# Kernel optimization log

Hardware: AMD Instinct MI355X
Metric: run time of the kernel (lower is better)

## Reference

```python
import jax, jax.numpy as jnp
import numpy as np
from jax import lax

C = 64      # embed_dim
DI = 128    # d_inner (expand=2)
N = 16      # d_state
RK = 4      # dt_rank = ceil(C/16)
K = 4       # scan directions
NB = 8      # total VSS blocks (4 stages x 2)


def conv2d(x, w, b, stride=1, pad=1, groups=1):
    y = lax.conv_general_dilated(x, w, (stride, stride), [(pad, pad), (pad, pad)],
                                 dimension_numbers=('NCHW', 'OIHW', 'NCHW'),
                                 feature_group_count=groups)
    return y + b[None, :, None, None]


def ln2d(x, g, b, eps=1e-6):
    xt = x.transpose(0, 2, 3, 1)
    mu = xt.mean(-1, keepdims=True)
    var = ((xt - mu) ** 2).mean(-1, keepdims=True)
    y = (xt - mu) / jnp.sqrt(var + eps) * g + b
    return y.transpose(0, 3, 1, 2)


def selective_scan(u, delta, A, Bm, Cm, D):
    # u, delta: (B,K,d,L); A: (K,d,n); Bm, Cm: (B,K,n,L); D: (K,d)
    dA = jnp.exp(delta[..., None] * A[None, :, :, None, :])               # (B,K,d,L,n)
    dBu = delta[..., None] * Bm.transpose(0, 1, 3, 2)[:, :, None] * u[..., None]

    def comb(c1, c2):
        a1, b1 = c1
        a2, b2 = c2
        return a2 * a1, a2 * b1 + b2

    _, h = lax.associative_scan(comb, (dA, dBu), axis=3)                  # (B,K,d,L,n)
    y = jnp.einsum('bkdln,bkln->bkdl', h, Cm.transpose(0, 1, 3, 2))
    return y + D[None, :, :, None] * u


def vss_block(x, lg, lb, inw, cw, cb, xpw, dtw, dtb, a_log, dp, ong, onb, outw):
    B, _, H, W = x.shape
    L = H * W
    h = ln2d(x, lg, lb)
    xz = jnp.einsum('bchw,ce->behw', h, inw)                              # (B,2*DI,H,W)
    xc, z = xz[:, :DI], xz[:, DI:]
    xc = jax.nn.silu(conv2d(xc, cw, cb, groups=DI))                       # depthwise 3x3
    x1 = xc.reshape(B, DI, L)                                             # row-major
    x2 = xc.transpose(0, 1, 3, 2).reshape(B, DI, L)                       # col-major
    xs = jnp.stack([x1, x2, x1[..., ::-1], x2[..., ::-1]], axis=1)        # (B,K,DI,L)
    xdbl = jnp.einsum('bkdl,krd->bkrl', xs, xpw)
    dts, Bs, Cs = xdbl[:, :, :RK], xdbl[:, :, RK:RK + N], xdbl[:, :, RK + N:]
    delta = jax.nn.softplus(jnp.einsum('bkrl,kdr->bkdl', dts, dtw) + dtb[None, :, :, None])
    A = -jnp.exp(a_log)
    ys = selective_scan(xs, delta, A, Bs, Cs, dp)                         # (B,K,DI,L)
    y = (ys[:, 0].reshape(B, DI, H, W)
         + ys[:, 1].reshape(B, DI, W, H).transpose(0, 1, 3, 2)
         + ys[:, 2, :, ::-1].reshape(B, DI, H, W)
         + ys[:, 3, :, ::-1].reshape(B, DI, W, H).transpose(0, 1, 3, 2))
    yt = y.transpose(0, 2, 3, 1)
    mu = yt.mean(-1, keepdims=True)
    var = ((yt - mu) ** 2).mean(-1, keepdims=True)
    yt = (yt - mu) / jnp.sqrt(var + 1e-6) * ong + onb
    yt = yt * jax.nn.silu(z.transpose(0, 2, 3, 1))
    out = jnp.einsum('bhwd,dc->bhwc', yt, outw).transpose(0, 3, 1, 2)
    return x + out


def setup_inputs() -> dict:
    key = jax.random.key(0)
    ks = jax.random.split(key, 16)
    nrm = lambda k, s, sc=0.02: jax.random.normal(k, s, jnp.float32) * sc
    return dict(
        E0=jax.random.uniform(ks[0], (1, 1, 256, 256), jnp.float32),
        pe_w=nrm(ks[1], (C, 1, 4, 4), 0.1),
        pe_b=jnp.zeros((C,), jnp.float32),
        pe_lg=jnp.ones((C,), jnp.float32),
        pe_lb=jnp.zeros((C,), jnp.float32),
        ln_g=jnp.ones((NB, C), jnp.float32),
        ln_b=jnp.zeros((NB, C), jnp.float32),
        in_w=nrm(ks[2], (NB, C, 2 * DI)),
        cv_w=nrm(ks[3], (NB, DI, 1, 3, 3), 0.1),
        cv_b=jnp.zeros((NB, DI), jnp.float32),
        xp_w=nrm(ks[4], (NB, K, RK + 2 * N, DI)),
        dt_w=nrm(ks[5], (NB, K, DI, RK)),
        dt_b=nrm(ks[6], (NB, K, DI), 0.5),
        A_log=jnp.broadcast_to(jnp.log(jnp.arange(1., N + 1)), (NB, K, DI, N)).astype(jnp.float32),
        Dp=jnp.ones((NB, K, DI), jnp.float32),
        on_g=jnp.ones((NB, DI), jnp.float32),
        on_b=jnp.zeros((NB, DI), jnp.float32),
        out_pw=nrm(ks[7], (NB, DI, C)),
        dn_w=nrm(ks[8], (3, C, C, 3, 3), 0.05),
        dn_b=jnp.zeros((3, C), jnp.float32),
        dn_g=jnp.ones((3, C), jnp.float32),
        dn_lb=jnp.zeros((3, C), jnp.float32),
        up_w=nrm(ks[9], (3, C, C, 3, 3), 0.05),
        up_b=jnp.zeros((3, C), jnp.float32),
        oc_w=nrm(ks[10], (C, C, 3, 3), 0.05),
        oc_b=jnp.zeros((C,), jnp.float32),
    )


def reference(E0, pe_w, pe_b, pe_lg, pe_lb, ln_g, ln_b, in_w, cv_w, cv_b, xp_w,
              dt_w, dt_b, A_log, Dp, on_g, on_b, out_pw, dn_w, dn_b, dn_g, dn_lb,
              up_w, up_b, oc_w, oc_b):
    x = conv2d(E0, pe_w, pe_b, stride=4, pad=0)
    x = ln2d(x, pe_lg, pe_lb)
    skips = []
    cur = 0
    for i in range(4):
        for _ in range(2):
            x = vss_block(x, ln_g[cur], ln_b[cur], in_w[cur], cv_w[cur], cv_b[cur],
                          xp_w[cur], dt_w[cur], dt_b[cur], A_log[cur], Dp[cur],
                          on_g[cur], on_b[cur], out_pw[cur])
            cur += 1
        skips.append(x)
        if i < 3:
            x = ln2d(conv2d(x, dn_w[i], dn_b[i], stride=2), dn_g[i], dn_lb[i])
    for i in range(3):
        Bq, Cq, Hq, Wq = x.shape
        x = jax.image.resize(x, (Bq, Cq, Hq * 2, Wq * 2), method='bilinear')
        x = jax.nn.silu(conv2d(x, up_w[i], up_b[i]))
        x = x + skips[-(i + 2)]
    Bq, Cq, Hq, Wq = x.shape
    x = jax.image.resize(x, (Bq, Cq, Hq * 4, Wq * 4), method='bilinear')
    x = jax.nn.silu(conv2d(x, oc_w, oc_b))
    return x
```

## Files before the change

kernel.cpp:

```cpp
#include <hip/hip_runtime.h>
#include <hip/hip_bf16.h>
#include <utility>

__global__ void k_patch_embed_ln(const float* __restrict__ E0, const float* __restrict__ w,
                                 const float* __restrict__ b, const float* __restrict__ g,
                                 const float* __restrict__ lb, float* __restrict__ out) {
  int p = blockIdx.x;
  int c = threadIdx.x;
  int oh = p >> 6, ow = p & 63;
  const float* src = E0 + (oh * 4) * 256 + ow * 4;
  const float* wc = w + c * 16;
  float acc = b[c];
#pragma unroll
  for (int i = 0; i < 4; i++)
#pragma unroll
    for (int j = 0; j < 4; j++) acc += src[i * 256 + j] * wc[i * 4 + j];
  float s = acc, s2 = acc * acc;
#pragma unroll
  for (int m = 32; m >= 1; m >>= 1) {
    s += __shfl_xor(s, m, 64);
    s2 += __shfl_xor(s2, m, 64);
  }
  float mu = s * (1.f / 64.f);
  float var = s2 * (1.f / 64.f) - mu * mu;
  float rstd = rsqrtf(var + 1e-6f);
  out[c * 4096 + p] = (acc - mu) * rstd * g[c] + lb[c];
}

__global__ void k_ln2d64(const float* __restrict__ x, const float* __restrict__ g,
                         const float* __restrict__ b, float* __restrict__ y, int HW) {
  int p = blockIdx.x;
  int c = threadIdx.x;
  float v = x[c * HW + p];
  float s = v, s2 = v * v;
#pragma unroll
  for (int m = 32; m >= 1; m >>= 1) {
    s += __shfl_xor(s, m, 64);
    s2 += __shfl_xor(s2, m, 64);
  }
  float mu = s * (1.f / 64.f);
  float var = s2 * (1.f / 64.f) - mu * mu;
  float rstd = rsqrtf(var + 1e-6f);
  y[c * HW + p] = (v - mu) * rstd * g[c] + b[c];
}

__global__ void k_lnproj(const float* __restrict__ x, const float* __restrict__ g,
                         const float* __restrict__ b, const float* __restrict__ w,
                         float* __restrict__ xc, float* __restrict__ z, int HW) {
  int p = blockIdx.x;
  int t = threadIdx.x;
  __shared__ float hsh[64];
  if (t < 64) {
    float v = x[t * HW + p];
    float s = v, s2 = v * v;
#pragma unroll
    for (int m = 32; m >= 1; m >>= 1) {
      s += __shfl_xor(s, m, 64);
      s2 += __shfl_xor(s2, m, 64);
    }
    float mu = s * (1.f / 64.f);
    float var = s2 * (1.f / 64.f) - mu * mu;
    float rstd = rsqrtf(var + 1e-6f);
    hsh[t] = (v - mu) * rstd * g[t] + b[t];
  }
  __syncthreads();
  float acc = 0.f;
  const float* wp = w + t;
#pragma unroll
  for (int c = 0; c < 64; c++) acc += hsh[c] * wp[c * 256];
  if (t < 128)
    xc[(size_t)p * 128 + t] = acc;
  else
    z[(size_t)p * 128 + (t - 128)] = acc;
}

__global__ void k_dwconv(const float* __restrict__ xc, const float* __restrict__ w,
                         const float* __restrict__ b, float* __restrict__ out, int H, int lgH) {
  int HW = H * H;
  int idx = blockIdx.x * blockDim.x + threadIdx.x;
  if (idx >= 128 * HW) return;
  int p = idx >> 7;
  int d = idx & 127;
  int ph = p >> lgH, pw = p & (H - 1);
  const float* wp = w + d * 9;
  float acc = b[d];
#pragma unroll
  for (int i = 0; i < 3; i++) {
    int ih = ph + i - 1;
    if (ih < 0 || ih >= H) continue;
#pragma unroll
    for (int j = 0; j < 3; j++) {
      int iw = pw + j - 1;
      if (iw < 0 || iw >= H) continue;
      acc += xc[(size_t)(ih * H + iw) * 128 + d] * wp[i * 3 + j];
    }
  }
  out[(size_t)p * 128 + d] = acc / (1.f + __expf(-acc));
}

__global__ void k_xproj(const float* __restrict__ xcs, const float* __restrict__ xpw,
                        const float* __restrict__ dtw, const float* __restrict__ dtb,
                        float* __restrict__ delta, float* __restrict__ Bs,
                        float* __restrict__ Cs, int H, int lgH) {
  int L = H * H;
  int l = blockIdx.x;
  int k = blockIdx.y;
  int t = threadIdx.x;
  int lm = (k & 2) ? (L - 1 - l) : l;
  int idx = (k & 1) ? ((lm & (H - 1)) * H + (lm >> lgH)) : lm;
  __shared__ float xs[128];
  __shared__ float part[36][4];
  __shared__ float r4[4];
  if (t < 128) xs[t] = xcs[(size_t)idx * 128 + t];
  __syncthreads();
  if (t < 144) {
    int r = t >> 2, q = t & 3;
    const float* wr = xpw + (k * 36 + r) * 128 + q * 32;
    const float* xp = xs + q * 32;
    float acc = 0.f;
#pragma unroll
    for (int c = 0; c < 32; c++) acc += xp[c] * wr[c];
    part[r][q] = acc;
  }
  __syncthreads();
  if (t < 36) {
    float acc = part[t][0] + part[t][1] + part[t][2] + part[t][3];
    if (t < 4)
      r4[t] = acc;
    else if (t < 20)
      Bs[((size_t)k * L + l) * 16 + (t - 4)] = acc;
    else
      Cs[((size_t)k * L + l) * 16 + (t - 20)] = acc;
  }
  __syncthreads();
  if (t < 128) {
    float dt = dtb[k * 128 + t];
    const float* wd = dtw + (k * 128 + t) * 4;
    dt += r4[0] * wd[0] + r4[1] * wd[1] + r4[2] * wd[2] + r4[3] * wd[3];
    float sp = fmaxf(dt, 0.f) + log1pf(__expf(-fabsf(dt)));
    delta[((size_t)k * L + l) * 128 + t] = sp;
  }
}

__global__ void k_scanA(const float* __restrict__ xcs, const float* __restrict__ delta,
                        const float* __restrict__ Bs, const float* __restrict__ A_log,
                        float* __restrict__ hloc, float* __restrict__ pA, int H, int lgH,
                        int nc, int cs) {
  int L = H * H;
  int c = blockIdx.x;
  int k = blockIdx.y;
  int d = threadIdx.x;
  float A[16], h[16];
#pragma unroll
  for (int n = 0; n < 16; n++) {
    A[n] = -expf(A_log[(k * 128 + d) * 16 + n]);
    h[n] = 0.f;
  }
  float sumdt = 0.f;
  int l0 = c * cs;
  for (int l = l0; l < l0 + cs; l++) {
    int lm = (k & 2) ? (L - 1 - l) : l;
    int idx = (k & 1) ? ((lm & (H - 1)) * H + (lm >> lgH)) : lm;
    float u = xcs[(size_t)idx * 128 + d];
    float dt = delta[((size_t)k * L + l) * 128 + d];
    float du = dt * u;
    sumdt += dt;
    const float4* bp = (const float4*)(Bs + ((size_t)k * L + l) * 16);
    float4 B0 = bp[0], B1 = bp[1], B2 = bp[2], B3 = bp[3];
    float Bv[16] = {B0.x, B0.y, B0.z, B0.w, B1.x, B1.y, B1.z, B1.w,
                    B2.x, B2.y, B2.z, B2.w, B3.x, B3.y, B3.z, B3.w};
#pragma unroll
    for (int n = 0; n < 16; n++) h[n] = __expf(dt * A[n]) * h[n] + Bv[n] * du;
  }
  size_t base = (((size_t)(k * 128 + d)) * nc + c) * 16;
#pragma unroll
  for (int n = 0; n < 16; n++) {
    hloc[base + n] = h[n];
    pA[base + n] = __expf(A[n] * sumdt);
  }
}

__global__ void k_scanB(const float* __restrict__ hloc, const float* __restrict__ pA,
                        float* __restrict__ hinit, int nc) {
  int tid = blockIdx.x * blockDim.x + threadIdx.x;
  int k = tid >> 11;
  int d = (tid >> 4) & 127;
  int n = tid & 15;
  size_t rb = ((size_t)(k * 128 + d)) * nc * 16 + n;
  float h = 0.f;
  for (int c = 0; c < nc; c++) {
    size_t a = rb + (size_t)c * 16;
    hinit[a] = h;
    h = pA[a] * h + hloc[a];
  }
}

__global__ void k_scanC(const float* __restrict__ xcs, const float* __restrict__ delta,
                        const float* __restrict__ Bs, const float* __restrict__ Cs,
                        const float* __restrict__ A_log, const float* __restrict__ Dp,
                        const float* __restrict__ hinit, float* __restrict__ ys, int H,
                        int lgH, int nc, int cs) {
  int L = H * H;
  int c = blockIdx.x;
  int k = blockIdx.y;
  int d = threadIdx.x;
  float A[16], h[16];
  size_t base = (((size_t)(k * 128 + d)) * nc + c) * 16;
#pragma unroll
  for (int n = 0; n < 16; n++) {
    A[n] = -expf(A_log[(k * 128 + d) * 16 + n]);
    h[n] = hinit[base + n];
  }
  float Dv = Dp[k * 128 + d];
  int l0 = c * cs;
  for (int l = l0; l < l0 + cs; l++) {
    int lm = (k & 2) ? (L - 1 - l) : l;
    int idx = (k & 1) ? ((lm & (H - 1)) * H + (lm >> lgH)) : lm;
    float u = xcs[(size_t)idx * 128 + d];
    float dt = delta[((size_t)k * L + l) * 128 + d];
    float du = dt * u;
    const float4* bp = (const float4*)(Bs + ((size_t)k * L + l) * 16);
    float4 B0 = bp[0], B1 = bp[1], B2 = bp[2], B3 = bp[3];
    float Bv[16] = {B0.x, B0.y, B0.z, B0.w, B1.x, B1.y, B1.z, B1.w,
                    B2.x, B2.y, B2.z, B2.w, B3.x, B3.y, B3.z, B3.w};
    const float4* cp = (const float4*)(Cs + ((size_t)k * L + l) * 16);
    float4 C0 = cp[0], C1 = cp[1], C2 = cp[2], C3 = cp[3];
    float Cv[16] = {C0.x, C0.y, C0.z, C0.w, C1.x, C1.y, C1.z, C1.w,
                    C2.x, C2.y, C2.z, C2.w, C3.x, C3.y, C3.z, C3.w};
    float y = 0.f;
#pragma unroll
    for (int n = 0; n < 16; n++) {
      h[n] = __expf(dt * A[n]) * h[n] + Bv[n] * du;
      y += h[n] * Cv[n];
    }
    ys[((size_t)k * L + l) * 128 + d] = y + Dv * u;
  }
}

__global__ void k_combine(const float* __restrict__ ys, const float* __restrict__ z,
                          const float* __restrict__ xin, const float* __restrict__ ong,
                          const float* __restrict__ onb, const float* __restrict__ outw,
                          float* __restrict__ xout, int H, int lgH) {
  int L = H * H;
  int p = blockIdx.x;
  int d = threadIdx.x;
  int ph = p >> lgH, pw = p & (H - 1);
  int l1 = pw * H + ph;
  float yv = ys[((size_t)0 * L + p) * 128 + d] + ys[((size_t)1 * L + l1) * 128 + d] +
             ys[((size_t)2 * L + (L - 1 - p)) * 128 + d] +
             ys[((size_t)3 * L + (L - 1 - l1)) * 128 + d];
  float s = yv, s2 = yv * yv;
#pragma unroll
  for (int m = 32; m >= 1; m >>= 1) {
    s += __shfl_xor(s, m, 64);
    s2 += __shfl_xor(s2, m, 64);
  }
  __shared__ float ws1[2], ws2[2];
  int wid = d >> 6;
  if ((d & 63) == 0) {
    ws1[wid] = s;
    ws2[wid] = s2;
  }
  __syncthreads();
  float tot = ws1[0] + ws1[1], tot2 = ws2[0] + ws2[1];
  float mu = tot * (1.f / 128.f);
  float var = tot2 * (1.f / 128.f) - mu * mu;
  float rstd = rsqrtf(var + 1e-6f);
  float zt = z[(size_t)p * 128 + d];
  float yt = ((yv - mu) * rstd * ong[d] + onb[d]) * (zt / (1.f + __expf(-zt)));
  __shared__ float ysm[128];
  ysm[d] = yt;
  __syncthreads();
  if (d < 64) {
    float acc = xin[(size_t)d * L + p];
#pragma unroll
    for (int q = 0; q < 128; q++) acc += ysm[q] * outw[q * 64 + d];
    xout[(size_t)d * L + p] = acc;
  }
}

__global__ void k_combine_lnproj(const float* __restrict__ ys, const float* __restrict__ z,
                                 const float* __restrict__ xin, const float* __restrict__ ong,
                                 const float* __restrict__ onb, const float* __restrict__ outw,
                                 const float* __restrict__ g2, const float* __restrict__ b2,
                                 const float* __restrict__ w2, float* __restrict__ xout,
                                 float* __restrict__ xc, float* __restrict__ zout, int H,
                                 int lgH) {
  int L = H * H;
  int p = blockIdx.x;
  int t = threadIdx.x;
  __shared__ float ysm[128], hnsh[64];
  __shared__ float ws1[2], ws2[2];
  float yv = 0.f;
  if (t < 128) {
    int ph = p >> lgH, pw = p & (H - 1);
    int l1 = pw * H + ph;
    yv = ys[((size_t)0 * L + p) * 128 + t] + ys[((size_t)1 * L + l1) * 128 + t] +
         ys[((size_t)2 * L + (L - 1 - p)) * 128 + t] +
         ys[((size_t)3 * L + (L - 1 - l1)) * 128 + t];
    float s = yv, s2 = yv * yv;
#pragma unroll
    for (int m = 32; m >= 1; m >>= 1) {
      s += __shfl_xor(s, m, 64);
      s2 += __shfl_xor(s2, m, 64);
    }
    if ((t & 63) == 0) {
      ws1[t >> 6] = s;
      ws2[t >> 6] = s2;
    }
  }
  __syncthreads();
  if (t < 128) {
    float tot = ws1[0] + ws1[1], tot2 = ws2[0] + ws2[1];
    float mu = tot * (1.f / 128.f);
    float var = tot2 * (1.f / 128.f) - mu * mu;
    float rstd = rsqrtf(var + 1e-6f);
    float zt = z[(size_t)p * 128 + t];
    ysm[t] = ((yv - mu) * rstd * ong[t] + onb[t]) * (zt / (1.f + __expf(-zt)));
  }
  __syncthreads();
  if (t < 64) {
    float acc = xin[(size_t)t * L + p];
#pragma unroll
    for (int q = 0; q < 128; q++) acc += ysm[q] * outw[q * 64 + t];
    xout[(size_t)t * L + p] = acc;
    float s = acc, s2 = acc * acc;
#pragma unroll
    for (int m = 32; m >= 1; m >>= 1) {
      s += __shfl_xor(s, m, 64);
      s2 += __shfl_xor(s2, m, 64);
    }
    float mu = s * (1.f / 64.f);
    float var = s2 * (1.f / 64.f) - mu * mu;
    float rstd = rsqrtf(var + 1e-6f);
    hnsh[t] = (acc - mu) * rstd * g2[t] + b2[t];
  }
  __syncthreads();
  float a2 = 0.f;
  const float* wp = w2 + t;
#pragma unroll
  for (int c = 0; c < 64; c++) a2 += hnsh[c] * wp[c * 256];
  if (t < 128)
    xc[(size_t)p * 128 + t] = a2;
  else
    zout[(size_t)p * 128 + (t - 128)] = a2;
}

__global__ void k_conv_naive(const float* __restrict__ x, const float* __restrict__ w,
                             const float* __restrict__ b, const float* __restrict__ skip,
                             float* __restrict__ out, int Hin, int Hout, int stride,
                             int do_silu) {
  int idx = blockIdx.x * blockDim.x + threadIdx.x;
  int HWo = Hout * Hout;
  if (idx >= 64 * HWo) return;
  int co = idx / HWo;
  int p = idx - co * HWo;
  int oh = p / Hout, ow = p - (p / Hout) * Hout;
  float acc = b[co];
  const float* wb = w + co * 64 * 9;
  for (int ci = 0; ci < 64; ci++) {
    const float* xb = x + (size_t)ci * Hin * Hin;
    const float* wc = wb + ci * 9;
#pragma unroll
    for (int i = 0; i < 3; i++) {
      int ih = oh * stride + i - 1;
      if (ih < 0 || ih >= Hin) continue;
#pragma unroll
      for (int j = 0; j < 3; j++) {
        int iw = ow * stride + j - 1;
        if (iw < 0 || iw >= Hin) continue;
        acc += xb[ih * Hin + iw] * wc[i * 3 + j];
      }
    }
  }
  if (do_silu) acc = acc / (1.f + __expf(-acc));
  if (skip) acc += skip[idx];
  out[idx] = acc;
}

__global__ void __launch_bounds__(256) k_conv16_up(const float* __restrict__ x,
                                                   const float* __restrict__ w,
                                                   const float* __restrict__ b,
                                                   float* __restrict__ out) {
  __shared__ __align__(16) float xsh[16][18][20];
  __shared__ __align__(16) float wsh[16][16][12];
  int t = threadIdx.x;
  int q = t & 63, cog = t >> 6;
  int qx = q & 7, qy = q >> 3;
  int ox = blockIdx.x * 16, oy = blockIdx.y * 16;
  int z16 = blockIdx.z * 16;
  float acc[4][4];
#pragma unroll
  for (int pp = 0; pp < 4; pp++)
#pragma unroll
    for (int i = 0; i < 4; i++) acc[pp][i] = 0.f;
  for (int cb = 0; cb < 64; cb += 16) {
    for (int i = t; i < 16 * 324; i += 256) {
      int ci = i / 324;
      int r = i - ci * 324;
      int iy = r / 18, ix = r - (r / 18) * 18;
      int gy = oy + iy - 1, gx = ox + ix - 1;
      float v = 0.f;
      if ((unsigned)gy < 256u && (unsigned)gx < 256u) {
        float sh = gy * 0.25f - 0.375f;
        float sw = gx * 0.25f - 0.375f;
        int h0 = (int)floorf(sh);
        float fh = sh - h0;
        int w0 = (int)floorf(sw);
        float fw = sw - w0;
        int h0c = max(h0, 0), h1c = min(h0 + 1, 63);
        int w0c = max(w0, 0), w1c = min(w0 + 1, 63);
        const float* xb = x + (size_t)(cb + ci) * 4096;
        v = (1.f - fh) * ((1.f - fw) * xb[h0c * 64 + w0c] + fw * xb[h0c * 64 + w1c]) +
            fh * ((1.f - fw) * xb[h1c * 64 + w0c] + fw * xb[h1c * 64 + w1c]);
      }
      xsh[ci][iy][ix] = v;
    }
    for (int i = t; i < 16 * 144; i += 256) {
      int ci = i / 144;
      int r = i - ci * 144;
      int col = r / 9, tap = r - (r / 9) * 9;
      wsh[ci][col][tap] = w[(size_t)(z16 + col) * 576 + (cb + ci) * 9 + tap];
    }
    __syncthreads();
#pragma unroll
    for (int ci = 0; ci < 16; ci++) {
      float xv[4][4];
#pragma unroll
      for (int r = 0; r < 4; r++) {
        float2 a = *(const float2*)&xsh[ci][2 * qy + r][2 * qx];
        float2 bq = *(const float2*)&xsh[ci][2 * qy + r][2 * qx + 2];
        xv[r][0] = a.x;
        xv[r][1] = a.y;
        xv[r][2] = bq.x;
        xv[r][3] = bq.y;
      }
#pragma unroll
      for (int i = 0; i < 4; i++) {
        int col = cog * 4 + i;
        float4 w0 = *(const float4*)&wsh[ci][col][0];
        float4 w1 = *(const float4*)&wsh[ci][col][4];
        float w8 = wsh[ci][col][8];
#pragma unroll
        for (int dy = 0; dy < 2; dy++)
#pragma unroll
          for (int dx = 0; dx < 2; dx++) {
            acc[dy * 2 + dx][i] += xv[dy + 0][dx + 0] * w0.x + xv[dy + 0][dx + 1] * w0.y +
                                   xv[dy + 0][dx + 2] * w0.z + xv[dy + 1][dx + 0] * w0.w +
                                   xv[dy + 1][dx + 1] * w1.x + xv[dy + 1][dx + 2] * w1.y +
                                   xv[dy + 2][dx + 0] * w1.z + xv[dy + 2][dx + 1] * w1.w +
                                   xv[dy + 2][dx + 2] * w8;
          }
      }
    }
    __syncthreads();
  }
#pragma unroll
  for (int dy = 0; dy < 2; dy++)
#pragma unroll
    for (int dx = 0; dx < 2; dx++) {
      int gy = oy + 2 * qy + dy, gx = ox + 2 * qx + dx;
#pragma unroll
      for (int i = 0; i < 4; i++) {
        int co = z16 + cog * 4 + i;
        float a = acc[dy * 2 + dx][i] + b[co];
        a = a / (1.f + __expf(-a));
        out[(size_t)co * 65536 + gy * 256 + gx] = a;
      }
    }
}

__global__ void k_resize(const float* __restrict__ x, float* __restrict__ out, int Hin,
                         int Win, int Hout, int Wout, float inv_scale) {
  int idx = blockIdx.x * blockDim.x + threadIdx.x;
  int HWo = Hout * Wout;
  if (idx >= 64 * HWo) return;
  int c = idx / HWo;
  int p = idx - c * HWo;
  int oh = p / Wout, ow = p - (p / Wout) * Wout;
  float sh = (oh + 0.5f) * inv_scale - 0.5f;
  float sw = (ow + 0.5f) * inv_scale - 0.5f;
  int h0 = (int)floorf(sh);
  float fh = sh - h0;
  int w0 = (int)floorf(sw);
  float fw = sw - w0;
  int h0c = min(max(h0, 0), Hin - 1), h1c = min(max(h0 + 1, 0), Hin - 1);
  int w0c = min(max(w0, 0), Win - 1), w1c = min(max(w0 + 1, 0), Win - 1);
  const float* xb = x + (size_t)c * Hin * Win;
  float v = (1.f - fh) * ((1.f - fw) * xb[h0c * Win + w0c] + fw * xb[h0c * Win + w1c]) +
            fh * ((1.f - fw) * xb[h1c * Win + w0c] + fw * xb[h1c * Win + w1c]);
  out[idx] = v;
}

extern "C" void kernel_launch(void* const* d_in, const int* in_sizes, int n_in, void* d_out,
                              int out_size, void* d_ws, size_t ws_size, hipStream_t stream) {
  const float* E0 = (const float*)d_in[0];
  const float* pe_w = (const float*)d_in[1];
  const float* pe_b = (const float*)d_in[2];
  const float* pe_lg = (const float*)d_in[3];
  const float* pe_lb = (const float*)d_in[4];
  const float* ln_g = (const float*)d_in[5];
  const float* ln_b = (const float*)d_in[6];
  const float* in_w = (const float*)d_in[7];
  const float* cv_w = (const float*)d_in[8];
  const float* cv_b = (const float*)d_in[9];
  const float* xp_w = (const float*)d_in[10];
  const float* dt_w = (const float*)d_in[11];
  const float* dt_b = (const float*)d_in[12];
  const float* A_log = (const float*)d_in[13];
  const float* Dp = (const float*)d_in[14];
  const float* on_g = (const float*)d_in[15];
  const float* on_b = (const float*)d_in[16];
  const float* out_pw = (const float*)d_in[17];
  const float* dn_w = (const float*)d_in[18];
  const float* dn_b = (const float*)d_in[19];
  const float* dn_g = (const float*)d_in[20];
  const float* dn_lb = (const float*)d_in[21];
  const float* up_w = (const float*)d_in[22];
  const float* up_b = (const float*)d_in[23];
  const float* oc_w = (const float*)d_in[24];
  const float* oc_b = (const float*)d_in[25];

  float* ws = (float*)d_ws;
  size_t off = 0;
  auto alloc = [&](size_t n) {
    float* p = ws + off;
    off += n;
    return p;
  };
  float* xA = alloc(64 * 4096);
  float* xB = alloc(64 * 4096);
  float* xc = alloc(128 * 4096);
  float* zb = alloc(128 * 4096);
  float* xcs = alloc(128 * 4096);
  float* dlt = alloc((size_t)4 * 128 * 4096);
  float* Bsb = alloc(4 * 16 * 4096);
  float* Csb = alloc(4 * 16 * 4096);
  float* ysb = alloc((size_t)4 * 128 * 4096);
  float* hloc = alloc((size_t)4 * 128 * 128 * 16);
  float* pAb = alloc((size_t)4 * 128 * 128 * 16);
  float* hin = alloc((size_t)4 * 128 * 128 * 16);
  float* sk0 = alloc(64 * 4096);
  float* sk1 = alloc(64 * 1024);
  float* sk2 = alloc(64 * 256);
  float* sk3 = alloc(64 * 64);
  float* tmpR = alloc((size_t)64 * 4096);

  k_patch_embed_ln<<<4096, 64, 0, stream>>>(E0, pe_w, pe_b, pe_lg, pe_lb, xB);
  float* x = xB;
  float* xalt = xA;

  int Hs[4] = {64, 32, 16, 8};
  int lgHs[4] = {6, 5, 4, 3};
  int CSs[4] = {32, 16, 8, 8};
  float* skips[4] = {sk0, sk1, sk2, sk3};
  int cur = 0;

  auto vss_core = [&](int H, int lgH, int cs) {
    int L = H * H;
    int nc = L / cs;
    k_dwconv<<<(128 * L + 255) / 256, 256, 0, stream>>>(xc, cv_w + (size_t)cur * 128 * 9,
                                                        cv_b + cur * 128, xcs, H, lgH);
    dim3 gx(L, 4);
    k_xproj<<<gx, 256, 0, stream>>>(xcs, xp_w + (size_t)cur * 4 * 36 * 128,
                                    dt_w + (size_t)cur * 4 * 128 * 4, dt_b + cur * 4 * 128,
                                    dlt, Bsb, Csb, H, lgH);
    const float* Al = A_log + (size_t)cur * 4 * 128 * 16;
    const float* Dv = Dp + cur * 4 * 128;
    dim3 ga(nc, 4);
    k_scanA<<<ga, 128, 0, stream>>>(xcs, dlt, Bsb, Al, hloc, pAb, H, lgH, nc, cs);
    k_scanB<<<32, 256, 0, stream>>>(hloc, pAb, hin, nc);
    k_scanC<<<ga, 128, 0, stream>>>(xcs, dlt, Bsb, Csb, Al, Dv, hin, ysb, H, lgH, nc, cs);
  };

  for (int i = 0; i < 4; i++) {
    int H = Hs[i], lgH = lgHs[i];
    int L = H * H;
    k_lnproj<<<L, 256, 0, stream>>>(x, ln_g + cur * 64, ln_b + cur * 64,
                                    in_w + (size_t)cur * 64 * 256, xc, zb, L);
    vss_core(H, lgH, CSs[i]);
    k_combine_lnproj<<<L, 256, 0, stream>>>(
        ysb, zb, x, on_g + cur * 128, on_b + cur * 128, out_pw + (size_t)cur * 128 * 64,
        ln_g + (cur + 1) * 64, ln_b + (cur + 1) * 64, in_w + (size_t)(cur + 1) * 64 * 256,
        xalt, xc, zb, H, lgH);
    std::swap(x, xalt);
    cur++;
    vss_core(H, lgH, CSs[i]);
    if (i < 3) {
      k_combine<<<L, 128, 0, stream>>>(ysb, zb, x, on_g + cur * 128, on_b + cur * 128,
                                       out_pw + (size_t)cur * 128 * 64, skips[i], H, lgH);
      cur++;
      int Ho = H / 2;
      k_conv_naive<<<(64 * Ho * Ho + 255) / 256, 256, 0, stream>>>(
          skips[i], dn_w + (size_t)i * 64 * 64 * 9, dn_b + i * 64, nullptr, xalt, H, Ho, 2, 0);
      k_ln2d64<<<Ho * Ho, 64, 0, stream>>>(xalt, dn_g + i * 64, dn_lb + i * 64, x, Ho * Ho);
    } else {
      k_combine<<<L, 128, 0, stream>>>(ysb, zb, x, on_g + cur * 128, on_b + cur * 128,
                                       out_pw + (size_t)cur * 128 * 64, xalt, H, lgH);
      std::swap(x, xalt);
      cur++;
    }
  }

  for (int i = 0; i < 3; i++) {
    int Hin = 8 << i, Ho = Hin * 2;
    k_resize<<<(64 * Ho * Ho + 255) / 256, 256, 0, stream>>>(x, tmpR, Hin, Hin, Ho, Ho, 0.5f);
    k_conv_naive<<<(64 * Ho * Ho + 255) / 256, 256, 0, stream>>>(
        tmpR, up_w + (size_t)i * 64 * 64 * 9, up_b + i * 64, skips[2 - i], xalt, Ho, Ho, 1, 1);
    std::swap(x, xalt);
  }

  dim3 gf(16, 16, 4);
  k_conv16_up<<<gf, 256, 0, stream>>>(x, oc_w, oc_b, (float*)d_out);
}
```

Before: 1.352 ms.

## Fuse x-projection into scan pass A and restructure final upsample conv

The per-position x-projection/softplus kernel is merged into the chunked scan pass A. Each block stages its chunk of inputs in shared memory, computes B, C and delta there and runs the local scan directly from shared memory, which removes a launch and the global round-trip of delta and B. The final 4x-upsample+conv kernel now stages a 6x6 source patch per channel and precomputes bilinear offsets and weights once. It also computes 32 output channels per block instead of 16, halving the grid. The trade-offs are fewer blocks, serial per-position syncs inside the fused kernel and more registers per thread in the conv.

Result: faster. 1.230 ms (-9.1%).

```diff
diff --git a/kernel.cpp b/kernel.cpp
--- a/kernel.cpp
+++ b/kernel.cpp
@@ -98,85 +98,100 @@
   out[(size_t)p * 128 + d] = acc / (1.f + __expf(-acc));
 }
 
-__global__ void k_xproj(const float* __restrict__ xcs, const float* __restrict__ xpw,
-                        const float* __restrict__ dtw, const float* __restrict__ dtb,
-                        float* __restrict__ delta, float* __restrict__ Bs,
-                        float* __restrict__ Cs, int H, int lgH) {
-  int L = H * H;
-  int l = blockIdx.x;
-  int k = blockIdx.y;
-  int t = threadIdx.x;
-  int lm = (k & 2) ? (L - 1 - l) : l;
-  int idx = (k & 1) ? ((lm & (H - 1)) * H + (lm >> lgH)) : lm;
-  __shared__ float xs[128];
-  __shared__ float part[36][4];
-  __shared__ float r4[4];
-  if (t < 128) xs[t] = xcs[(size_t)idx * 128 + t];
-  __syncthreads();
-  if (t < 144) {
-    int r = t >> 2, q = t & 3;
-    const float* wr = xpw + (k * 36 + r) * 128 + q * 32;
-    const float* xp = xs + q * 32;
-    float acc = 0.f;
-#pragma unroll
-    for (int c = 0; c < 32; c++) acc += xp[c] * wr[c];
-    part[r][q] = acc;
-  }
-  __syncthreads();
-  if (t < 36) {
-    float acc = part[t][0] + part[t][1] + part[t][2] + part[t][3];
-    if (t < 4)
-      r4[t] = acc;
-    else if (t < 20)
-      Bs[((size_t)k * L + l) * 16 + (t - 4)] = acc;
-    else
-      Cs[((size_t)k * L + l) * 16 + (t - 20)] = acc;
-  }
-  __syncthreads();
-  if (t < 128) {
-    float dt = dtb[k * 128 + t];
-    const float* wd = dtw + (k * 128 + t) * 4;
-    dt += r4[0] * wd[0] + r4[1] * wd[1] + r4[2] * wd[2] + r4[3] * wd[3];
-    float sp = fmaxf(dt, 0.f) + log1pf(__expf(-fabsf(dt)));
-    delta[((size_t)k * L + l) * 128 + t] = sp;
-  }
-}
-
-__global__ void k_scanA(const float* __restrict__ xcs, const float* __restrict__ delta,
-                        const float* __restrict__ Bs, const float* __restrict__ A_log,
-                        float* __restrict__ hloc, float* __restrict__ pA, int H, int lgH,
-                        int nc, int cs) {
+__global__ void __launch_bounds__(256) k_xproj_scanA(
+    const float* __restrict__ xcs, const float* __restrict__ xpw,
+    const float* __restrict__ dtw, const float* __restrict__ dtb,
+    const float* __restrict__ A_log, float* __restrict__ delta, float* __restrict__ Bs,
+    float* __restrict__ Cs, float* __restrict__ hloc, float* __restrict__ pA, int H,
+    int lgH, int nc, int cs) {
   int L = H * H;
   int c = blockIdx.x;
   int k = blockIdx.y;
-  int d = threadIdx.x;
-  float A[16], h[16];
-#pragma unroll
-  for (int n = 0; n < 16; n++) {
-    A[n] = -expf(A_log[(k * 128 + d) * 16 + n]);
-    h[n] = 0.f;
-  }
-  float sumdt = 0.f;
+  int t = threadIdx.x;
   int l0 = c * cs;
-  for (int l = l0; l < l0 + cs; l++) {
+  __shared__ float xs[32][128];
+  __shared__ float dsh[32][128];
+  __shared__ float Bsh[32][16];
+  __shared__ float r4s[4];
+  for (int i = t; i < cs * 128; i += 256) {
+    int j = i >> 7, d = i & 127;
+    int l = l0 + j;
     int lm = (k & 2) ? (L - 1 - l) : l;
     int idx = (k & 1) ? ((lm & (H - 1)) * H + (lm >> lgH)) : lm;
-    float u = xcs[(size_t)idx * 128 + d];
-    float dt = delta[((size_t)k * L + l) * 128 + d];
-    float du = dt * u;
-    sumdt += dt;
-    const float4* bp = (const float4*)(Bs + ((size_t)k * L + l) * 16);
-    float4 B0 = bp[0], B1 = bp[1], B2 = bp[2], B3 = bp[3];
-    float Bv[16] = {B0.x, B0.y, B0.z, B0.w, B1.x, B1.y, B1.z, B1.w,
-                    B2.x, B2.y, B2.z, B2.w, B3.x, B3.y, B3.z, B3.w};
-#pragma unroll
-    for (int n = 0; n < 16; n++) h[n] = __expf(dt * A[n]) * h[n] + Bv[n] * du;
-  }
-  size_t base = (((size_t)(k * 128 + d)) * nc + c) * 16;
-#pragma unroll
-  for (int n = 0; n < 16; n++) {
-    hloc[base + n] = h[n];
-    pA[base + n] = __expf(A[n] * sumdt);
+    xs[j][d] = xcs[(size_t)idx * 128 + d];
+  }
+  int r = t >> 2, q = t & 3;
+  float4 wreg[8];
+  if (t < 144) {
+    const float4* wp = (const float4*)(xpw + (size_t)(k * 36 + r) * 128 + q * 32);
+#pragma unroll
+    for (int m = 0; m < 8; m++) wreg[m] = wp[m];
+  }
+  float4 dtw4 = {0, 0, 0, 0};
+  float dtbv = 0.f;
+  if (t < 128) {
+    dtw4 = *(const float4*)(dtw + (size_t)(k * 128 + t) * 4);
+    dtbv = dtb[k * 128 + t];
+  }
+  __syncthreads();
+  for (int j = 0; j < cs; j++) {
+    if (t < 144) {
+      const float4* xp = (const float4*)&xs[j][q * 32];
+      float a = 0.f;
+#pragma unroll
+      for (int m = 0; m < 8; m++) {
+        float4 xv = xp[m];
+        a += xv.x * wreg[m].x + xv.y * wreg[m].y + xv.z * wreg[m].z + xv.w * wreg[m].w;
+      }
+      a += __shfl_xor(a, 1);
+      a += __shfl_xor(a, 2);
+      if (q == 0) {
+        int l = l0 + j;
+        if (r < 4)
+          r4s[r] = a;
+        else if (r < 20) {
+          Bsh[j][r - 4] = a;
+          Bs[((size_t)k * L + l) * 16 + (r - 4)] = a;
+        } else
+          Cs[((size_t)k * L + l) * 16 + (r - 20)] = a;
+      }
+    }
+    __syncthreads();
+    if (t < 128) {
+      float dt = dtbv + r4s[0] * dtw4.x + r4s[1] * dtw4.y + r4s[2] * dtw4.z + r4s[3] * dtw4.w;
+      float sp = fmaxf(dt, 0.f) + log1pf(__expf(-fabsf(dt)));
+      dsh[j][t] = sp;
+      delta[((size_t)k * L + (l0 + j)) * 128 + t] = sp;
+    }
+    __syncthreads();
+  }
+  if (t < 128) {
+    int d = t;
+    float A[16], h[16];
+#pragma unroll
+    for (int n = 0; n < 16; n++) {
+      A[n] = -__expf(A_log[(size_t)(k * 128 + d) * 16 + n]);
+      h[n] = 0.f;
+    }
+    float sumdt = 0.f;
+    for (int j = 0; j < cs; j++) {
+      float u = xs[j][d];
+      float dt = dsh[j][d];
+      float du = dt * u;
+      sumdt += dt;
+      const float4* bp = (const float4*)Bsh[j];
+      float4 B0 = bp[0], B1 = bp[1], B2 = bp[2], B3 = bp[3];
+      float Bv[16] = {B0.x, B0.y, B0.z, B0.w, B1.x, B1.y, B1.z, B1.w,
+                      B2.x, B2.y, B2.z, B2.w, B3.x, B3.y, B3.z, B3.w};
+#pragma unroll
+      for (int n = 0; n < 16; n++) h[n] = __expf(dt * A[n]) * h[n] + Bv[n] * du;
+    }
+    size_t base = (((size_t)(k * 128 + d)) * nc + c) * 16;
+#pragma unroll
+    for (int n = 0; n < 16; n++) {
+      hloc[base + n] = h[n];
+      pA[base + n] = __expf(A[n] * sumdt);
+    }
   }
 }
 
@@ -208,7 +223,7 @@
   size_t base = (((size_t)(k * 128 + d)) * nc + c) * 16;
 #pragma unroll
   for (int n = 0; n < 16; n++) {
-    A[n] = -expf(A_log[(k * 128 + d) * 16 + n]);
+    A[n] = -__expf(A_log[(size_t)(k * 128 + d) * 16 + n]);
     h[n] = hinit[base + n];
   }
   float Dv = Dp[k * 128 + d];
@@ -382,49 +397,71 @@
                                                    const float* __restrict__ w,
                                                    const float* __restrict__ b,
                                                    float* __restrict__ out) {
-  __shared__ __align__(16) float xsh[16][18][20];
-  __shared__ __align__(16) float wsh[16][16][12];
+  __shared__ float ssh[64][36];
+  __shared__ float pfh[324], pfw[324];
+  __shared__ int poff[324];
+  __shared__ __align__(16) float xsh[8][18][20];
+  __shared__ __align__(16) float wsh[8][32][12];
   int t = threadIdx.x;
   int q = t & 63, cog = t >> 6;
   int qx = q & 7, qy = q >> 3;
   int ox = blockIdx.x * 16, oy = blockIdx.y * 16;
-  int z16 = blockIdx.z * 16;
-  float acc[4][4];
+  int z32 = blockIdx.z * 32;
+  int sy0 = (oy >> 2) - 1, sx0 = (ox >> 2) - 1;
+  for (int i = t; i < 64 * 36; i += 256) {
+    int ci = i / 36;
+    int rr = i - ci * 36;
+    int ry = rr / 6, cc = rr - ry * 6;
+    int sy = min(max(sy0 + ry, 0), 63);
+    int sx = min(max(sx0 + cc, 0), 63);
+    ssh[ci][rr] = x[(size_t)ci * 4096 + sy * 64 + sx];
+  }
+  for (int i = t; i < 324; i += 256) {
+    int iy = i / 18, ix = i - iy * 18;
+    int gy = oy + iy - 1, gx = ox + ix - 1;
+    if ((unsigned)gy < 256u && (unsigned)gx < 256u) {
+      float sh = gy * 0.25f - 0.375f;
+      float sw = gx * 0.25f - 0.375f;
+      int h0 = (int)floorf(sh), w0 = (int)floorf(sw);
+      pfh[i] = sh - h0;
+      pfw[i] = sw - w0;
+      poff[i] = (h0 - sy0) * 6 + (w0 - sx0);
+    } else {
+      poff[i] = -1;
+      pfh[i] = 0.f;
+      pfw[i] = 0.f;
+    }
+  }
+  float acc[4][8];
 #pragma unroll
   for (int pp = 0; pp < 4; pp++)
 #pragma unroll
-    for (int i = 0; i < 4; i++) acc[pp][i] = 0.f;
-  for (int cb = 0; cb < 64; cb += 16) {
-    for (int i = t; i < 16 * 324; i += 256) {
+    for (int i = 0; i < 8; i++) acc[pp][i] = 0.f;
+  __syncthreads();
+  for (int cb = 0; cb < 64; cb += 8) {
+    for (int i = t; i < 8 * 324; i += 256) {
       int ci = i / 324;
-      int r = i - ci * 324;
-      int iy = r / 18, ix = r - (r / 18) * 18;
-      int gy = oy + iy - 1, gx = ox + ix - 1;
+      int rdx = i - ci * 324;
+      int off = poff[rdx];
       float v = 0.f;
-      if ((unsigned)gy < 256u && (unsigned)gx < 256u) {
-        float sh = gy * 0.25f - 0.375f;
-        float sw = gx * 0.25f - 0.375f;
-        int h0 = (int)floorf(sh);
-        float fh = sh - h0;
-        int w0 = (int)floorf(sw);
-        float fw = sw - w0;
-        int h0c = max(h0, 0), h1c = min(h0 + 1, 63);
-        int w0c = max(w0, 0), w1c = min(w0 + 1, 63);
-        const float* xb = x + (size_t)(cb + ci) * 4096;
-        v = (1.f - fh) * ((1.f - fw) * xb[h0c * 64 + w0c] + fw * xb[h0c * 64 + w1c]) +
-            fh * ((1.f - fw) * xb[h1c * 64 + w0c] + fw * xb[h1c * 64 + w1c]);
+      if (off >= 0) {
+        float fh = pfh[rdx], fw = pfw[rdx];
+        const float* s = &ssh[cb + ci][off];
+        v = (1.f - fh) * ((1.f - fw) * s[0] + fw * s[1]) +
+            fh * ((1.f - fw) * s[6] + fw * s[7]);
       }
-      xsh[ci][iy][ix] = v;
-    }
-    for (int i = t; i < 16 * 144; i += 256) {
-      int ci = i / 144;
-      int r = i - ci * 144;
-      int col = r / 9, tap = r - (r / 9) * 9;
-      wsh[ci][col][tap] = w[(size_t)(z16 + col) * 576 + (cb + ci) * 9 + tap];
+      int iy = rdx / 18;
+      xsh[ci][iy][rdx - iy * 18] = v;
+    }
+    for (int i = t; i < 8 * 288; i += 256) {
+      int ci = i / 288;
+      int rr = i - ci * 288;
+      int col = rr / 9, tap = rr - col * 9;
+      wsh[ci][col][tap] = w[(size_t)(z32 + col) * 576 + (cb + ci) * 9 + tap];
     }
     __syncthreads();
 #pragma unroll
-    for (int ci = 0; ci < 16; ci++) {
+    for (int ci = 0; ci < 8; ci++) {
       float xv[4][4];
 #pragma unroll
       for (int r = 0; r < 4; r++) {
@@ -436,20 +473,20 @@
         xv[r][3] = bq.y;
       }
 #pragma unroll
-      for (int i = 0; i < 4; i++) {
-        int col = cog * 4 + i;
-        float4 w0 = *(const float4*)&wsh[ci][col][0];
-        float4 w1 = *(const float4*)&wsh[ci][col][4];
-        float w8 = wsh[ci][col][8];
+      for (int i = 0; i < 8; i++) {
+        int col = cog * 8 + i;
+        float4 w0v = *(const float4*)&wsh[ci][col][0];
+        float4 w1v = *(const float4*)&wsh[ci][col][4];
+        float w8v = wsh[ci][col][8];
 #pragma unroll
         for (int dy = 0; dy < 2; dy++)
 #pragma unroll
           for (int dx = 0; dx < 2; dx++) {
-            acc[dy * 2 + dx][i] += xv[dy + 0][dx + 0] * w0.x + xv[dy + 0][dx + 1] * w0.y +
-                                   xv[dy + 0][dx + 2] * w0.z + xv[dy + 1][dx + 0] * w0.w +
-                                   xv[dy + 1][dx + 1] * w1.x + xv[dy + 1][dx + 2] * w1.y +
-                                   xv[dy + 2][dx + 0] * w1.z + xv[dy + 2][dx + 1] * w1.w +
-                                   xv[dy + 2][dx + 2] * w8;
+            acc[dy * 2 + dx][i] += xv[dy + 0][dx + 0] * w0v.x + xv[dy + 0][dx + 1] * w0v.y +
+                                   xv[dy + 0][dx + 2] * w0v.z + xv[dy + 1][dx + 0] * w0v.w +
+                                   xv[dy + 1][dx + 1] * w1v.x + xv[dy + 1][dx + 2] * w1v.y +
+                                   xv[dy + 2][dx + 0] * w1v.z + xv[dy + 2][dx + 1] * w1v.w +
+                                   xv[dy + 2][dx + 2] * w8v;
           }
       }
     }
@@ -461,8 +498,8 @@
     for (int dx = 0; dx < 2; dx++) {
       int gy = oy + 2 * qy + dy, gx = ox + 2 * qx + dx;
 #pragma unroll
-      for (int i = 0; i < 4; i++) {
-        int co = z16 + cog * 4 + i;
+      for (int i = 0; i < 8; i++) {
+        int co = z32 + cog * 8 + i;
         float a = acc[dy * 2 + dx][i] + b[co];
         a = a / (1.f + __expf(-a));
         out[(size_t)co * 65536 + gy * 256 + gx] = a;
@@ -561,16 +598,16 @@
     int nc = L / cs;
     k_dwconv<<<(128 * L + 255) / 256, 256, 0, stream>>>(xc, cv_w + (size_t)cur * 128 * 9,
                                                         cv_b + cur * 128, xcs, H, lgH);
-    dim3 gx(L, 4);
-    k_xproj<<<gx, 256, 0, stream>>>(xcs, xp_w + (size_t)cur * 4 * 36 * 128,
-                                    dt_w + (size_t)cur * 4 * 128 * 4, dt_b + cur * 4 * 128,
-                                    dlt, Bsb, Csb, H, lgH);
     const float* Al = A_log + (size_t)cur * 4 * 128 * 16;
     const float* Dv = Dp + cur * 4 * 128;
     dim3 ga(nc, 4);
-    k_scanA<<<ga, 128, 0, stream>>>(xcs, dlt, Bsb, Al, hloc, pAb, H, lgH, nc, cs);
+    k_xproj_scanA<<<ga, 256, 0, stream>>>(xcs, xp_w + (size_t)cur * 4 * 36 * 128,
+                                          dt_w + (size_t)cur * 4 * 128 * 4,
+                                          dt_b + cur * 4 * 128, Al, dlt, Bsb, Csb, hloc,
+                                          pAb, H, lgH, nc, cs);
     k_scanB<<<32, 256, 0, stream>>>(hloc, pAb, hin, nc);
-    k_scanC<<<ga, 128, 0, stream>>>(xcs, dlt, Bsb, Csb, Al, Dv, hin, ysb, H, lgH, nc, cs);
+    dim3 gc(nc, 4);
+    k_scanC<<<gc, 128, 0, stream>>>(xcs, dlt, Bsb, Csb, Al, Dv, hin, ysb, H, lgH, nc, cs);
   };
 
   for (int i = 0; i < 4; i++) {
@@ -610,6 +647,6 @@
     std::swap(x, xalt);
   }
 
-  dim3 gf(16, 16, 4);
+  dim3 gf(16, 16, 2);
   k_conv16_up<<<gf, 256, 0, stream>>>(x, oc_w, oc_b, (float*)d_out);
 }
```
